# Performance work log

Measured on AMD Instinct MI355X. Metric: run time of the kernel, lower is better.

The kernel has to match this reference:

```python
import jax, jax.numpy as jnp
import numpy as np

N = 50000       # num nodes
F_IN = 256      # num_features
HID = 128       # num_hidden
E = 800000      # structural edges (no self loops)
E_KNN = 500000  # knn edges (no self loops)


def setup_inputs() -> dict:
    rng = np.random.default_rng(0)
    # loop-free random edges: col != row guaranteed
    row = rng.integers(0, N, E)
    col = (row + 1 + rng.integers(0, N - 1, E)) % N
    edge_index = jnp.asarray(np.stack([row, col]), dtype=jnp.int32)
    rowk = rng.integers(0, N, E_KNN)
    colk = (rowk + 1 + rng.integers(0, N - 1, E_KNN)) % N
    knn_graph = jnp.asarray(np.stack([rowk, colk]), dtype=jnp.int32)

    key = jax.random.key(0)
    ks = jax.random.split(key, 8)
    x = jax.random.normal(ks[0], (N, F_IN), dtype=jnp.float32)
    s = 1.0 / np.sqrt(F_IN)  # nn.Linear default init range
    def lin(kw, kb):
        W = jax.random.uniform(kw, (HID, F_IN), minval=-s, maxval=s, dtype=jnp.float32)
        b = jax.random.uniform(kb, (HID,), minval=-s, maxval=s, dtype=jnp.float32)
        return W, b
    W_s1, b_s1 = lin(ks[1], ks[2])
    W_s2, b_s2 = lin(ks[3], ks[4])
    W_f2, b_f2 = lin(ks[5], ks[6])
    return {"x": x, "edge_index": edge_index, "knn_graph": knn_graph,
            "W_s1": W_s1, "b_s1": b_s1, "W_s2": W_s2, "b_s2": b_s2,
            "W_f2": W_f2, "b_f2": b_f2}


def _gcn_norm(edge_index, num_nodes):
    # add_remaining_self_loops on loop-free input == append all self loops (w=1)
    loop = jnp.arange(num_nodes, dtype=edge_index.dtype)
    row = jnp.concatenate([edge_index[0], loop])
    col = jnp.concatenate([edge_index[1], loop])
    w = jnp.ones(row.shape[0], dtype=jnp.float32)
    deg = jax.ops.segment_sum(w, col, num_segments=num_nodes)
    dinv = jnp.where(deg > 0, jax.lax.rsqrt(deg), 0.0)
    return row, col, dinv[row] * w * dinv[col]


def _gcn(x, W, b, row, col, norm, K):
    # eval mode: dropout(p=0.6) is identity
    h = x @ W.T + b
    n = x.shape[0]
    for _ in range(K):
        # gather source feats -> edge-weight scale -> scatter-add to targets (SpMM)
        h = jax.ops.segment_sum(norm[:, None] * h[row], col, num_segments=n)
    return h


def reference(x, edge_index, knn_graph, W_s1, b_s1, W_s2, b_s2, W_f2, b_f2):
    n = x.shape[0]
    r, c, nm = _gcn_norm(edge_index, n)
    rk, ck, nmk = _gcn_norm(knn_graph, n)
    h0 = _gcn(x, W_s1, b_s1, r, c, nm, 2)
    h1 = _gcn(x, W_s2, b_s2, r, c, nm, 10)
    z0 = _gcn(x, W_f2, b_f2, r, c, nm, 2)
    # original computes gcn_f2(x, edge_index, K=2) twice; in eval mode both equal z0
    z1 = z0 + _gcn(x, W_f2, b_f2, rk, ck, nmk, 1)
    return (h0, h1, z0, z1)
```

## Files before the change

### kernel.cpp

```cpp
#include <hip/hip_runtime.h>
#include <hip/hip_fp16.h>

#define F_IN 256
#define HID 128

typedef _Float16 half8 __attribute__((ext_vector_type(8)));
typedef _Float16 half4v __attribute__((ext_vector_type(4)));
typedef float f32x4 __attribute__((ext_vector_type(4)));


__global__ void k_count2(const int* __restrict__ col_s, int E, int* __restrict__ cnt_s,
                         const int* __restrict__ col_k, int EK, int* __restrict__ cnt_k) {
  int e = blockIdx.x * blockDim.x + threadIdx.x;
  if (e < E) {
    atomicAdd(&cnt_s[col_s[e]], 1);
  } else {
    int f = e - E;
    if (f < EK) atomicAdd(&cnt_k[col_k[f]], 1);
  }
}

__global__ void k_scan_block(const int* __restrict__ in, int n, int* __restrict__ out,
                             int* __restrict__ bsum) {
  __shared__ int s[1024];
  int tid = threadIdx.x;
  int i = blockIdx.x * 1024 + tid;
  int v = (i < n) ? in[i] : 0;
  s[tid] = v;
  __syncthreads();
  for (int off = 1; off < 1024; off <<= 1) {
    int t = (tid >= off) ? s[tid - off] : 0;
    __syncthreads();
    s[tid] += t;
    __syncthreads();
  }
  if (i < n) out[i] = s[tid] - v;
  if (tid == 1023) bsum[blockIdx.x] = s[1023];
}

__global__ void k_scan_single(int* __restrict__ bsum, int nb, int* __restrict__ tail) {
  if (threadIdx.x == 0 && blockIdx.x == 0) {
    int run = 0;
    for (int b = 0; b < nb; ++b) { int t = bsum[b]; bsum[b] = run; run += t; }
    *tail = run;
  }
}

__global__ void k_add_off(int* __restrict__ out, const int* __restrict__ bsum, int n) {
  int i = blockIdx.x * blockDim.x + threadIdx.x;
  if (i < n) out[i] += bsum[i >> 10];
}

__global__ void k_scatter2(const int* __restrict__ row_s, const int* __restrict__ col_s, int E,
                           const int* __restrict__ offs_s, int* __restrict__ cur_s,
                           int* __restrict__ csr_s,
                           const int* __restrict__ row_k, const int* __restrict__ col_k, int EK,
                           const int* __restrict__ offs_k, int* __restrict__ cur_k,
                           int* __restrict__ csr_k) {
  int e = blockIdx.x * blockDim.x + threadIdx.x;
  if (e < E) {
    int c = col_s[e];
    int p = offs_s[c] + atomicAdd(&cur_s[c], 1);
    csr_s[p] = row_s[e];
  } else {
    int f = e - E;
    if (f < EK) {
      int c = col_k[f];
      int p = offs_k[c] + atomicAdd(&cur_k[c], 1);
      csr_k[p] = row_k[f];
    }
  }
}


__global__ void k_cvt_w(const float* __restrict__ W0, const float* __restrict__ W1,
                        const float* __restrict__ W2, _Float16* __restrict__ Wh) {
  const int sz = HID * F_IN;
  int idx = (blockIdx.x * 256 + threadIdx.x) * 4;
  const float* src = (idx < sz) ? (W0 + idx)
                   : (idx < 2 * sz) ? (W1 + idx - sz)
                   : (W2 + idx - 2 * sz);
  float4 v = *(const float4*)src;
  half4v o;
  o[0] = (_Float16)v.x; o[1] = (_Float16)v.y; o[2] = (_Float16)v.z; o[3] = (_Float16)v.w;
  *(half4v*)(Wh + idx) = o;
}


__global__ __launch_bounds__(256, 4) void k_gemm3(
    const float* __restrict__ x, const _Float16* __restrict__ Wh,
    const float* __restrict__ b0, const float* __restrict__ b1, const float* __restrict__ b2,
    int n, const int* __restrict__ cnt_s, const int* __restrict__ cnt_k,
    _Float16* __restrict__ gS1, _Float16* __restrict__ gS2,
    _Float16* __restrict__ gF2s, _Float16* __restrict__ gF2k)
{
  int w = blockIdx.y;
  int lane = threadIdx.x & 63;
  int wv = threadIdx.x >> 6;
  int l15 = lane & 15, lhi = lane >> 4;
  int mrow = blockIdx.x * 64 + wv * 16 + l15;
  bool mok = mrow < n;
  int arow = mok ? mrow : (n - 1);

  const float* bias = (w == 0) ? b0 : (w == 1) ? b1 : b2;
  _Float16* dst = (w == 0) ? gS1 : (w == 1) ? gS2 : gF2s;
  const _Float16* Wp = Wh + (size_t)w * HID * F_IN + (size_t)l15 * F_IN + lhi * 8;
  const float* xr = x + (size_t)arow * F_IN + lhi * 8;

  f32x4 acc[8];
#pragma unroll
  for (int nt = 0; nt < 8; ++nt) {
    float4 bv = *(const float4*)(bias + nt * 16 + lhi * 4);
    acc[nt] = (f32x4){bv.x, bv.y, bv.z, bv.w};
  }

#pragma unroll
  for (int kt = 0; kt < 8; ++kt) {
    float4 lo = *(const float4*)(xr + kt * 32);
    float4 hi = *(const float4*)(xr + kt * 32 + 4);
    half8 av;
    av[0] = (_Float16)lo.x; av[1] = (_Float16)lo.y; av[2] = (_Float16)lo.z; av[3] = (_Float16)lo.w;
    av[4] = (_Float16)hi.x; av[5] = (_Float16)hi.y; av[6] = (_Float16)hi.z; av[7] = (_Float16)hi.w;
#pragma unroll
    for (int nt = 0; nt < 8; ++nt) {
      half8 bf = *(const half8*)(Wp + (size_t)nt * 16 * F_IN + kt * 32);
      acc[nt] = __builtin_amdgcn_mfma_f32_16x16x32_f16(bf, av, acc[nt], 0, 0, 0);
    }
  }

  if (mok) {
    float ss = rsqrtf((float)(cnt_s[mrow] + 1));
    float sk = (w == 2) ? rsqrtf((float)(cnt_k[mrow] + 1)) : 0.f;
#pragma unroll
    for (int nt = 0; nt < 8; ++nt) {
      int nbase = nt * 16 + lhi * 4;
      half4v o;
      o[0] = (_Float16)(acc[nt][0] * ss); o[1] = (_Float16)(acc[nt][1] * ss);
      o[2] = (_Float16)(acc[nt][2] * ss); o[3] = (_Float16)(acc[nt][3] * ss);
      *(half4v*)(dst + (size_t)mrow * HID + nbase) = o;
      if (w == 2) {
        half4v o2;
        o2[0] = (_Float16)(acc[nt][0] * sk); o2[1] = (_Float16)(acc[nt][1] * sk);
        o2[2] = (_Float16)(acc[nt][2] * sk); o2[3] = (_Float16)(acc[nt][3] * sk);
        *(half4v*)(gF2k + (size_t)mrow * HID + nbase) = o2;
      }
    }
  }
}


__device__ inline float2 h2f2(unsigned int u) {
  __half2 h; *(unsigned int*)&h = u; return __half22float2(h);
}

__device__ inline void spmm_store(void* out, size_t base, float2 acc, float deg, int mode,
                                  const float2* __restrict__ add) {
  if (mode == 0) {
    float sc = 1.0f / deg;
    __half2 h = __float22half2_rn(make_float2(acc.x * sc, acc.y * sc));
    ((__half2*)out)[base] = h;
  } else {
    float sc = rsqrtf(deg);
    float2 o = make_float2(acc.x * sc, acc.y * sc);
    if (mode == 2) { float2 z = add[base]; o.x += z.x; o.y += z.y; }
    ((float2*)out)[base] = o;
  }
}

__global__ __launch_bounds__(256) void k_spmm_h(
    const unsigned int* __restrict__ gin, void* __restrict__ gout,
    const int* __restrict__ csr, const int* __restrict__ offs, const int* __restrict__ cnt,
    int n, int mode, const float2* __restrict__ addsrc)
{
  int w = (blockIdx.x << 2) | ((int)threadIdx.x >> 6);
  if (w >= n) return;
  int lane = threadIdx.x & 63;
  int beg = offs[w], end = offs[w + 1];
  size_t base = (size_t)w * 64 + lane;
  float2 acc = h2f2(gin[base]);
  int e = beg;
#pragma unroll 1
  for (; e + 16 <= end; e += 16) {
    unsigned int u[16];
#pragma unroll
    for (int j = 0; j < 16; ++j)
      u[j] = gin[((size_t)(unsigned)csr[e + j] << 6) + lane];
    float sx = 0.f, sy = 0.f;
#pragma unroll
    for (int j = 0; j < 16; ++j) { float2 v = h2f2(u[j]); sx += v.x; sy += v.y; }
    acc.x += sx; acc.y += sy;
  }
#pragma unroll 1
  for (; e + 4 <= end; e += 4) {
    unsigned int u[4];
#pragma unroll
    for (int j = 0; j < 4; ++j)
      u[j] = gin[((size_t)(unsigned)csr[e + j] << 6) + lane];
    float sx = 0.f, sy = 0.f;
#pragma unroll
    for (int j = 0; j < 4; ++j) { float2 v = h2f2(u[j]); sx += v.x; sy += v.y; }
    acc.x += sx; acc.y += sy;
  }
  for (; e < end; ++e) {
    float2 v = h2f2(gin[((size_t)(unsigned)csr[e] << 6) + lane]);
    acc.x += v.x; acc.y += v.y;
  }
  spmm_store(gout, base, acc, (float)(cnt[w] + 1), mode, addsrc);
}

__global__ __launch_bounds__(256) void k_spmm3(
    const unsigned int* __restrict__ g0, const unsigned int* __restrict__ g1,
    const unsigned int* __restrict__ g2,
    void* __restrict__ o0, void* __restrict__ o1, void* __restrict__ o2,
    int md0, int md1, int md2,
    const int* __restrict__ csr, const int* __restrict__ offs, const int* __restrict__ cnt,
    int n)
{
  int w = (blockIdx.x << 2) | ((int)threadIdx.x >> 6);
  if (w >= n) return;
  int lane = threadIdx.x & 63;
  int beg = offs[w], end = offs[w + 1];
  size_t base = (size_t)w * 64 + lane;
  float2 a0 = h2f2(g0[base]), a1 = h2f2(g1[base]), a2 = h2f2(g2[base]);
  int e = beg;
#pragma unroll 1
  for (; e + 4 <= end; e += 4) {
    size_t s[4];
#pragma unroll
    for (int j = 0; j < 4; ++j) s[j] = ((size_t)(unsigned)csr[e + j] << 6) + lane;
    unsigned int u0[4], u1[4], u2[4];
#pragma unroll
    for (int j = 0; j < 4; ++j) { u0[j] = g0[s[j]]; u1[j] = g1[s[j]]; u2[j] = g2[s[j]]; }
#pragma unroll
    for (int j = 0; j < 4; ++j) {
      float2 v;
      v = h2f2(u0[j]); a0.x += v.x; a0.y += v.y;
      v = h2f2(u1[j]); a1.x += v.x; a1.y += v.y;
      v = h2f2(u2[j]); a2.x += v.x; a2.y += v.y;
    }
  }
  for (; e < end; ++e) {
    size_t s0 = ((size_t)(unsigned)csr[e] << 6) + lane;
    float2 v;
    v = h2f2(g0[s0]); a0.x += v.x; a0.y += v.y;
    v = h2f2(g1[s0]); a1.x += v.x; a1.y += v.y;
    v = h2f2(g2[s0]); a2.x += v.x; a2.y += v.y;
  }
  float deg = (float)(cnt[w] + 1);
  spmm_store(o0, base, a0, deg, md0, nullptr);
  spmm_store(o1, base, a1, deg, md1, nullptr);
  spmm_store(o2, base, a2, deg, md2, nullptr);
}


extern "C" void kernel_launch(void* const* d_in, const int* in_sizes, int n_in,
                              void* d_out, int out_size, void* d_ws, size_t ws_size,
                              hipStream_t stream) {
  const float* x    = (const float*)d_in[0];
  const int*   ei   = (const int*)d_in[1];
  const int*   knn  = (const int*)d_in[2];
  const float* W_s1 = (const float*)d_in[3];
  const float* b_s1 = (const float*)d_in[4];
  const float* W_s2 = (const float*)d_in[5];
  const float* b_s2 = (const float*)d_in[6];
  const float* W_f2 = (const float*)d_in[7];
  const float* b_f2 = (const float*)d_in[8];

  const int N  = in_sizes[0] / F_IN;
  const int E  = in_sizes[1] / 2;
  const int EK = in_sizes[2] / 2;
  const int* row_s = ei;   const int* col_s = ei + E;
  const int* row_k = knn;  const int* col_k = knn + EK;

  char* p = (char*)d_ws;
  auto carve = [&](size_t bytes) {
    char* r = p; p += (bytes + 511) & ~(size_t)511; return (void*)r;
  };
  int* cnt_s = (int*)carve((size_t)N * 4);
  int* cnt_k = (int*)carve((size_t)N * 4);
  int* cur_s = (int*)carve((size_t)N * 4);
  int* cur_k = (int*)carve((size_t)N * 4);
  char* zero_end = p;
  int* offs_s = (int*)carve((size_t)(N + 1) * 4);
  int* offs_k = (int*)carve((size_t)(N + 1) * 4);
  int* bsum   = (int*)carve(4096);
  int* csr_s  = (int*)carve((size_t)E * 4);
  int* csr_k  = (int*)carve((size_t)EK * 4);
  _Float16* Wh  = (_Float16*)carve((size_t)3 * HID * F_IN * 2);
  _Float16* gS1 = (_Float16*)carve((size_t)N * HID * 2);
  _Float16* gS2 = (_Float16*)carve((size_t)N * HID * 2);
  _Float16* gF2s= (_Float16*)carve((size_t)N * HID * 2);
  _Float16* gF2k= (_Float16*)carve((size_t)N * HID * 2);
  _Float16* tS2 = (_Float16*)carve((size_t)N * HID * 2);

  float* out_h0 = (float*)d_out;
  float* out_h1 = out_h0 + (size_t)N * HID;
  float* out_z0 = out_h1 + (size_t)N * HID;
  float* out_z1 = out_z0 + (size_t)N * HID;
  _Float16* tS1 = (_Float16*)out_z1;
  _Float16* tF2 = tS1 + (size_t)N * HID;

  hipMemsetAsync(d_ws, 0, (size_t)(zero_end - (char*)d_ws), stream);

  const int tpb = 256;
  int etot = E + EK;
  k_count2<<<(etot + tpb - 1) / tpb, tpb, 0, stream>>>(col_s, E, cnt_s, col_k, EK, cnt_k);

  int nb = (N + 1023) / 1024;
  k_scan_block<<<nb, 1024, 0, stream>>>(cnt_s, N, offs_s, bsum);
  k_scan_single<<<1, 64, 0, stream>>>(bsum, nb, offs_s + N);
  k_add_off<<<(N + tpb - 1) / tpb, tpb, 0, stream>>>(offs_s, bsum, N);
  k_scan_block<<<nb, 1024, 0, stream>>>(cnt_k, N, offs_k, bsum);
  k_scan_single<<<1, 64, 0, stream>>>(bsum, nb, offs_k + N);
  k_add_off<<<(N + tpb - 1) / tpb, tpb, 0, stream>>>(offs_k, bsum, N);

  k_scatter2<<<(etot + tpb - 1) / tpb, tpb, 0, stream>>>(
      row_s, col_s, E, offs_s, cur_s, csr_s,
      row_k, col_k, EK, offs_k, cur_k, csr_k);

  k_cvt_w<<<96, 256, 0, stream>>>(W_s1, W_s2, W_f2, Wh);
  dim3 ggrid((N + 63) / 64, 3);
  k_gemm3<<<ggrid, 256, 0, stream>>>(x, Wh, b_s1, b_s2, b_f2, N, cnt_s, cnt_k,
                                     gS1, gS2, gF2s, gF2k);

  int spmm_grid = (N + 3) / 4;

  k_spmm3<<<spmm_grid, 256, 0, stream>>>((const unsigned int*)gS1, (const unsigned int*)gS2,
                                         (const unsigned int*)gF2s,
                                         tS1, tS2, tF2, 0, 0, 0,
                                         csr_s, offs_s, cnt_s, N);
  k_spmm3<<<spmm_grid, 256, 0, stream>>>((const unsigned int*)tS1, (const unsigned int*)tS2,
                                         (const unsigned int*)tF2,
                                         out_h0, gS1, out_z0, 1, 0, 1,
                                         csr_s, offs_s, cnt_s, N);

  {
    _Float16* cur = gS1; _Float16* alt = tS2;
    for (int it = 0; it < 7; ++it) {
      k_spmm_h<<<spmm_grid, 256, 0, stream>>>((const unsigned int*)cur, alt,
                                              csr_s, offs_s, cnt_s, N, 0, nullptr);
      _Float16* t = cur; cur = alt; alt = t;
    }
    k_spmm_h<<<spmm_grid, 256, 0, stream>>>((const unsigned int*)cur, out_h1,
                                            csr_s, offs_s, cnt_s, N, 1, nullptr);
  }

  k_spmm_h<<<spmm_grid, 256, 0, stream>>>((const unsigned int*)gF2k, out_z1,
                                          csr_k, offs_k, cnt_k, N, 2,
                                          (const float2*)out_z0);
}
```

Baseline: 723.4 us.

## Stage x tile in swizzled LDS once and compute all three weight GEMMs per block

The GEMM kernel now converts a 64-row tile of x to fp16 once into XOR-swizzled shared memory. Each block loops over all three weight matrices, so x is read from global memory once instead of three times. Each wave now covers 32 output columns for all 64 rows rather than 16 rows by all 128 columns, reusing weight fragments across four row tiles. This adds 32 KB of LDS per block and a serial loop over weights, which lowers occupancy and cuts the grid to a third.

```diff
diff --git a/kernel.cpp b/kernel.cpp
--- a/kernel.cpp
+++ b/kernel.cpp
@@ -94,55 +94,94 @@
     _Float16* __restrict__ gS1, _Float16* __restrict__ gS2,
     _Float16* __restrict__ gF2s, _Float16* __restrict__ gF2k)
 {
-  int w = blockIdx.y;
-  int lane = threadIdx.x & 63;
-  int wv = threadIdx.x >> 6;
+  __shared__ _Float16 xs[64 * F_IN];
+  int tid = threadIdx.x;
+  int m0 = blockIdx.x * 64;
+
+  {
+    int r = tid >> 2;
+    int cbase = (tid & 3) * 64;
+    int gr = m0 + r; if (gr >= n) gr = n - 1;
+    const float* src = x + (size_t)gr * F_IN + cbase;
+    unsigned sw = (unsigned)((r & 7) << 4);
+    char* drow = (char*)xs + r * (F_IN * 2) + cbase * 2;
+#pragma unroll
+    for (int i = 0; i < 8; ++i) {
+      float4 a = *(const float4*)(src + i * 8);
+      float4 b = *(const float4*)(src + i * 8 + 4);
+      half8 v;
+      v[0] = (_Float16)a.x; v[1] = (_Float16)a.y; v[2] = (_Float16)a.z; v[3] = (_Float16)a.w;
+      v[4] = (_Float16)b.x; v[5] = (_Float16)b.y; v[6] = (_Float16)b.z; v[7] = (_Float16)b.w;
+      *(half8*)(drow + (((unsigned)(i * 16)) ^ sw)) = v;
+    }
+  }
+  __syncthreads();
+
+  int lane = tid & 63;
+  int wv = tid >> 6;
   int l15 = lane & 15, lhi = lane >> 4;
-  int mrow = blockIdx.x * 64 + wv * 16 + l15;
-  bool mok = mrow < n;
-  int arow = mok ? mrow : (n - 1);
-
-  const float* bias = (w == 0) ? b0 : (w == 1) ? b1 : b2;
-  _Float16* dst = (w == 0) ? gS1 : (w == 1) ? gS2 : gF2s;
-  const _Float16* Wp = Wh + (size_t)w * HID * F_IN + (size_t)l15 * F_IN + lhi * 8;
-  const float* xr = x + (size_t)arow * F_IN + lhi * 8;
-
-  f32x4 acc[8];
-#pragma unroll
-  for (int nt = 0; nt < 8; ++nt) {
-    float4 bv = *(const float4*)(bias + nt * 16 + lhi * 4);
-    acc[nt] = (f32x4){bv.x, bv.y, bv.z, bv.w};
-  }
-
-#pragma unroll
-  for (int kt = 0; kt < 8; ++kt) {
-    float4 lo = *(const float4*)(xr + kt * 32);
-    float4 hi = *(const float4*)(xr + kt * 32 + 4);
-    half8 av;
-    av[0] = (_Float16)lo.x; av[1] = (_Float16)lo.y; av[2] = (_Float16)lo.z; av[3] = (_Float16)lo.w;
-    av[4] = (_Float16)hi.x; av[5] = (_Float16)hi.y; av[6] = (_Float16)hi.z; av[7] = (_Float16)hi.w;
-#pragma unroll
-    for (int nt = 0; nt < 8; ++nt) {
-      half8 bf = *(const half8*)(Wp + (size_t)nt * 16 * F_IN + kt * 32);
-      acc[nt] = __builtin_amdgcn_mfma_f32_16x16x32_f16(bf, av, acc[nt], 0, 0, 0);
-    }
-  }
-
-  if (mok) {
-    float ss = rsqrtf((float)(cnt_s[mrow] + 1));
-    float sk = (w == 2) ? rsqrtf((float)(cnt_k[mrow] + 1)) : 0.f;
-#pragma unroll
-    for (int nt = 0; nt < 8; ++nt) {
-      int nbase = nt * 16 + lhi * 4;
-      half4v o;
-      o[0] = (_Float16)(acc[nt][0] * ss); o[1] = (_Float16)(acc[nt][1] * ss);
-      o[2] = (_Float16)(acc[nt][2] * ss); o[3] = (_Float16)(acc[nt][3] * ss);
-      *(half4v*)(dst + (size_t)mrow * HID + nbase) = o;
-      if (w == 2) {
-        half4v o2;
-        o2[0] = (_Float16)(acc[nt][0] * sk); o2[1] = (_Float16)(acc[nt][1] * sk);
-        o2[2] = (_Float16)(acc[nt][2] * sk); o2[3] = (_Float16)(acc[nt][3] * sk);
-        *(half4v*)(gF2k + (size_t)mrow * HID + nbase) = o2;
+  unsigned swr = (unsigned)((l15 & 7) << 4);
+
+  float ss[4], sk[4];
+  int nodes[4];
+#pragma unroll
+  for (int m = 0; m < 4; ++m) {
+    int node = m0 + m * 16 + l15;
+    nodes[m] = node;
+    int cn = (node < n) ? node : (n - 1);
+    ss[m] = rsqrtf((float)(cnt_s[cn] + 1));
+    sk[m] = rsqrtf((float)(cnt_k[cn] + 1));
+  }
+
+  for (int w = 0; w < 3; ++w) {
+    const float* bias = (w == 0) ? b0 : (w == 1) ? b1 : b2;
+    _Float16* dst = (w == 0) ? gS1 : (w == 1) ? gS2 : gF2s;
+    const _Float16* Wp = Wh + (size_t)w * HID * F_IN
+                            + (size_t)(wv * 32 + l15) * F_IN + lhi * 8;
+
+    f32x4 acc[4][2];
+#pragma unroll
+    for (int n2 = 0; n2 < 2; ++n2) {
+      float4 bv = *(const float4*)(bias + wv * 32 + n2 * 16 + lhi * 4);
+      f32x4 b4 = {bv.x, bv.y, bv.z, bv.w};
+#pragma unroll
+      for (int m = 0; m < 4; ++m) acc[m][n2] = b4;
+    }
+
+#pragma unroll
+    for (int kt = 0; kt < 8; ++kt) {
+      half8 wf[2];
+#pragma unroll
+      for (int n2 = 0; n2 < 2; ++n2)
+        wf[n2] = *(const half8*)(Wp + (size_t)n2 * 16 * F_IN + kt * 32);
+      half8 xf[4];
+      unsigned coff = ((unsigned)((lhi * 8 + kt * 32) * 2)) ^ swr;
+#pragma unroll
+      for (int m = 0; m < 4; ++m)
+        xf[m] = *(const half8*)((const char*)xs + (m * 16 + l15) * (F_IN * 2) + coff);
+#pragma unroll
+      for (int m = 0; m < 4; ++m)
+#pragma unroll
+        for (int n2 = 0; n2 < 2; ++n2)
+          acc[m][n2] = __builtin_amdgcn_mfma_f32_16x16x32_f16(wf[n2], xf[m], acc[m][n2], 0, 0, 0);
+    }
+
+#pragma unroll
+    for (int m = 0; m < 4; ++m) {
+      if (nodes[m] >= n) continue;
+      size_t obase = (size_t)nodes[m] * HID + wv * 32 + lhi * 4;
+#pragma unroll
+      for (int n2 = 0; n2 < 2; ++n2) {
+        half4v o;
+        o[0] = (_Float16)(acc[m][n2][0] * ss[m]); o[1] = (_Float16)(acc[m][n2][1] * ss[m]);
+        o[2] = (_Float16)(acc[m][n2][2] * ss[m]); o[3] = (_Float16)(acc[m][n2][3] * ss[m]);
+        *(half4v*)(dst + obase + n2 * 16) = o;
+        if (w == 2) {
+          half4v o2;
+          o2[0] = (_Float16)(acc[m][n2][0] * sk[m]); o2[1] = (_Float16)(acc[m][n2][1] * sk[m]);
+          o2[2] = (_Float16)(acc[m][n2][2] * sk[m]); o2[3] = (_Float16)(acc[m][n2][3] * sk[m]);
+          *(half4v*)(gF2k + obase + n2 * 16) = o2;
+        }
       }
     }
   }
@@ -319,9 +358,8 @@
       row_k, col_k, EK, offs_k, cur_k, csr_k);
 
   k_cvt_w<<<96, 256, 0, stream>>>(W_s1, W_s2, W_f2, Wh);
-  dim3 ggrid((N + 63) / 64, 3);
-  k_gemm3<<<ggrid, 256, 0, stream>>>(x, Wh, b_s1, b_s2, b_f2, N, cnt_s, cnt_k,
-                                     gS1, gS2, gF2s, gF2k);
+  k_gemm3<<<(N + 63) / 64, 256, 0, stream>>>(x, Wh, b_s1, b_s2, b_f2, N, cnt_s, cnt_k,
+                                             gS1, gS2, gF2s, gF2k);
 
   int spmm_grid = (N + 3) / 4;
 
```

Measured after the change: 719.6 us. No clear change (-0.5%).

## Stage x tile in shared memory once and loop all three weights per block

Applied to the files above, without the earlier changes.

The GEMM kernel now loads a 32-row tile of x into LDS as fp16 (with an XOR swizzle to avoid bank conflicts) and computes all three weight projections from it. Before, each of three grid slices re-read x from global memory and converted it. The kernel also splits the N dimension across wave pairs and raises the occupancy hint. This is meant to cut redundant global reads of x, at the cost of an LDS barrier and more serialized work per block.

```diff
diff --git a/kernel.cpp b/kernel.cpp
--- a/kernel.cpp
+++ b/kernel.cpp
@@ -87,62 +87,90 @@
 }
 
 
-__global__ __launch_bounds__(256, 4) void k_gemm3(
+__global__ __launch_bounds__(256, 8) void k_gemm3(
     const float* __restrict__ x, const _Float16* __restrict__ Wh,
     const float* __restrict__ b0, const float* __restrict__ b1, const float* __restrict__ b2,
     int n, const int* __restrict__ cnt_s, const int* __restrict__ cnt_k,
     _Float16* __restrict__ gS1, _Float16* __restrict__ gS2,
     _Float16* __restrict__ gF2s, _Float16* __restrict__ gF2k)
 {
-  int w = blockIdx.y;
-  int lane = threadIdx.x & 63;
-  int wv = threadIdx.x >> 6;
+  __shared__ _Float16 xs[32 * F_IN];
+  int tid = threadIdx.x;
+  int m0 = blockIdx.x * 32;
+
+  {
+    int r = tid >> 3;
+    int cbase = (tid & 7) * 32;
+    int gr = m0 + r; if (gr >= n) gr = n - 1;
+    const float* src = x + (size_t)gr * F_IN + cbase;
+    unsigned sw = (unsigned)((r & 7) << 4);
+    char* drow = (char*)xs + r * (F_IN * 2);
+#pragma unroll
+    for (int i = 0; i < 4; ++i) {
+      float4 a = *(const float4*)(src + i * 8);
+      float4 b = *(const float4*)(src + i * 8 + 4);
+      half8 v;
+      v[0] = (_Float16)a.x; v[1] = (_Float16)a.y; v[2] = (_Float16)a.z; v[3] = (_Float16)a.w;
+      v[4] = (_Float16)b.x; v[5] = (_Float16)b.y; v[6] = (_Float16)b.z; v[7] = (_Float16)b.w;
+      *(half8*)(drow + (((unsigned)(cbase * 2 + i * 16)) ^ sw)) = v;
+    }
+  }
+  __syncthreads();
+
+  int lane = tid & 63;
+  int wv = tid >> 6;
+  int mh = wv >> 1, ch = wv & 1;
   int l15 = lane & 15, lhi = lane >> 4;
-  int mrow = blockIdx.x * 64 + wv * 16 + l15;
-  bool mok = mrow < n;
-  int arow = mok ? mrow : (n - 1);
-
-  const float* bias = (w == 0) ? b0 : (w == 1) ? b1 : b2;
-  _Float16* dst = (w == 0) ? gS1 : (w == 1) ? gS2 : gF2s;
-  const _Float16* Wp = Wh + (size_t)w * HID * F_IN + (size_t)l15 * F_IN + lhi * 8;
-  const float* xr = x + (size_t)arow * F_IN + lhi * 8;
-
-  f32x4 acc[8];
-#pragma unroll
-  for (int nt = 0; nt < 8; ++nt) {
-    float4 bv = *(const float4*)(bias + nt * 16 + lhi * 4);
-    acc[nt] = (f32x4){bv.x, bv.y, bv.z, bv.w};
-  }
-
-#pragma unroll
-  for (int kt = 0; kt < 8; ++kt) {
-    float4 lo = *(const float4*)(xr + kt * 32);
-    float4 hi = *(const float4*)(xr + kt * 32 + 4);
-    half8 av;
-    av[0] = (_Float16)lo.x; av[1] = (_Float16)lo.y; av[2] = (_Float16)lo.z; av[3] = (_Float16)lo.w;
-    av[4] = (_Float16)hi.x; av[5] = (_Float16)hi.y; av[6] = (_Float16)hi.z; av[7] = (_Float16)hi.w;
-#pragma unroll
-    for (int nt = 0; nt < 8; ++nt) {
-      half8 bf = *(const half8*)(Wp + (size_t)nt * 16 * F_IN + kt * 32);
-      acc[nt] = __builtin_amdgcn_mfma_f32_16x16x32_f16(bf, av, acc[nt], 0, 0, 0);
-    }
-  }
-
-  if (mok) {
-    float ss = rsqrtf((float)(cnt_s[mrow] + 1));
-    float sk = (w == 2) ? rsqrtf((float)(cnt_k[mrow] + 1)) : 0.f;
-#pragma unroll
-    for (int nt = 0; nt < 8; ++nt) {
-      int nbase = nt * 16 + lhi * 4;
-      half4v o;
-      o[0] = (_Float16)(acc[nt][0] * ss); o[1] = (_Float16)(acc[nt][1] * ss);
-      o[2] = (_Float16)(acc[nt][2] * ss); o[3] = (_Float16)(acc[nt][3] * ss);
-      *(half4v*)(dst + (size_t)mrow * HID + nbase) = o;
+  int rloc = mh * 16 + l15;
+  unsigned swr = (unsigned)((rloc & 7) << 4);
+  const char* xrow = (const char*)xs + rloc * (F_IN * 2);
+
+  int node = m0 + rloc;
+  int cn = (node < n) ? node : (n - 1);
+  float ss = rsqrtf((float)(cnt_s[cn] + 1));
+  float sk = rsqrtf((float)(cnt_k[cn] + 1));
+
+#pragma unroll 1
+  for (int w = 0; w < 3; ++w) {
+    const float* bias = (w == 0) ? b0 : (w == 1) ? b1 : b2;
+    _Float16* dst = (w == 0) ? gS1 : (w == 1) ? gS2 : gF2s;
+    const _Float16* Wp = Wh + (size_t)w * HID * F_IN
+                            + (size_t)(ch * 64 + l15) * F_IN + lhi * 8;
+
+    f32x4 acc[4];
+#pragma unroll
+    for (int nt = 0; nt < 4; ++nt) {
+      float4 bv = *(const float4*)(bias + ch * 64 + nt * 16 + lhi * 4);
+      acc[nt] = (f32x4){bv.x, bv.y, bv.z, bv.w};
+    }
+
+#pragma unroll
+    for (int kt = 0; kt < 8; ++kt) {
+      half8 xf = *(const half8*)(xrow + (((unsigned)((kt * 32 + lhi * 8) * 2)) ^ swr));
+#pragma unroll
+      for (int nt = 0; nt < 4; ++nt) {
+        half8 wf = *(const half8*)(Wp + (size_t)nt * 16 * F_IN + kt * 32);
+        acc[nt] = __builtin_amdgcn_mfma_f32_16x16x32_f16(wf, xf, acc[nt], 0, 0, 0);
+      }
+    }
+
+    if (node < n) {
+      size_t obase = (size_t)node * HID + ch * 64 + lhi * 4;
+#pragma unroll
+      for (int nt = 0; nt < 4; ++nt) {
+        half4v o;
+        o[0] = (_Float16)(acc[nt][0] * ss); o[1] = (_Float16)(acc[nt][1] * ss);
+        o[2] = (_Float16)(acc[nt][2] * ss); o[3] = (_Float16)(acc[nt][3] * ss);
+        *(half4v*)(dst + obase + nt * 16) = o;
+      }
       if (w == 2) {
-        half4v o2;
-        o2[0] = (_Float16)(acc[nt][0] * sk); o2[1] = (_Float16)(acc[nt][1] * sk);
-        o2[2] = (_Float16)(acc[nt][2] * sk); o2[3] = (_Float16)(acc[nt][3] * sk);
-        *(half4v*)(gF2k + (size_t)mrow * HID + nbase) = o2;
+#pragma unroll
+        for (int nt = 0; nt < 4; ++nt) {
+          half4v o2;
+          o2[0] = (_Float16)(acc[nt][0] * sk); o2[1] = (_Float16)(acc[nt][1] * sk);
+          o2[2] = (_Float16)(acc[nt][2] * sk); o2[3] = (_Float16)(acc[nt][3] * sk);
+          *(half4v*)(gF2k + obase + nt * 16) = o2;
+        }
       }
     }
   }
@@ -319,9 +347,8 @@
       row_k, col_k, EK, offs_k, cur_k, csr_k);
 
   k_cvt_w<<<96, 256, 0, stream>>>(W_s1, W_s2, W_f2, Wh);
-  dim3 ggrid((N + 63) / 64, 3);
-  k_gemm3<<<ggrid, 256, 0, stream>>>(x, Wh, b_s1, b_s2, b_f2, N, cnt_s, cnt_k,
-                                     gS1, gS2, gF2s, gF2k);
+  k_gemm3<<<(N + 31) / 32, 256, 0, stream>>>(x, Wh, b_s1, b_s2, b_f2, N, cnt_s, cnt_k,
+                                             gS1, gS2, gF2s, gF2k);
 
   int spmm_grid = (N + 3) / 4;
 
```

After: 725.8 us. About the same (+0.3%).
